# Kernel optimization log

Measured on AMD Instinct MI355X. Metric: run time of the kernel, lower is better.

Reference implementation:

```python
import jax, jax.numpy as jnp
import numpy as np

N = 262144
FEAT = 128
HID = 256


def setup_inputs() -> dict:
    key = jax.random.key(0)
    ks = jax.random.split(key, 6)
    rotation = jax.random.normal(ks[0], (N, 3, 3), dtype=jnp.float32)
    feature = jax.random.normal(ks[1], (N, FEAT), dtype=jnp.float32)
    # MLP params (scaled like default init)
    W1 = jax.random.normal(ks[2], (FEAT, HID), dtype=jnp.float32) / np.sqrt(FEAT)
    b1 = jnp.zeros((HID,), dtype=jnp.float32)
    W2 = jax.random.normal(ks[3], (HID, HID), dtype=jnp.float32) / np.sqrt(HID)
    b2 = jnp.zeros((HID,), dtype=jnp.float32)
    W3 = jax.random.normal(ks[4], (HID, 9), dtype=jnp.float32) / np.sqrt(HID)
    b3 = jnp.zeros((9,), dtype=jnp.float32)
    return {"rotation": rotation, "feature": feature,
            "W1": W1, "b1": b1, "W2": W2, "b2": b2, "W3": W3, "b3": b3}


def _mlp(feature, W1, b1, W2, b2, W3, b3):
    h = jax.nn.relu(feature @ W1 + b1)
    h = jax.nn.relu(h @ W2 + b2)
    return h @ W3 + b3  # [N, 9]


def reference(rotation, feature, W1, b1, W2, b2, W3, b3):
    # mat = net(feature).reshape(-1,3,3) + I
    mat = _mlp(feature, W1, b1, W2, b2, W3, b3).reshape(-1, 3, 3) + jnp.eye(3, dtype=rotation.dtype)
    # new_mat = mat @ rotation, then Procrustes projection via SVD: U @ V^T
    new_mat = jnp.einsum('nab,nbc->nac', mat, rotation)
    U, S, Vh = jnp.linalg.svd(new_mat, full_matrices=False)
    out = jnp.einsum('nab,nbc->nac', U, Vh)  # torch: U @ V.T == U @ Vh
    logdet = jnp.zeros((rotation.shape[0],), dtype=rotation.dtype)
    return out, logdet
```

## Files before the change

kernel.cpp:

```cpp
#include <hip/hip_runtime.h>
#include <math.h>


#define N_ROWS 262144
#define FEAT   128
#define HID    256
#define TM     64
#define NT     256
#define NBLK   (N_ROWS/TM)

typedef _Float16 h8v __attribute__((ext_vector_type(8)));
typedef float    f4v __attribute__((ext_vector_type(4)));

#define WS_W1H 0
#define WS_W1L 65536
#define WS_W2H 131072
#define WS_W2L 262144

#define OFF_AH  0
#define OFF_AL  16384
#define OFF_H1H 0
#define OFF_H1L 32768
#define W3SEC   2320
#define OFF_W3  65536
#define OFF_B3  (OFF_W3 + 4*W3SEC)
#define OFF_RS  (OFF_B3 + 64)
#define OFF_MS  (OFF_RS + TM*12*4)
#define SMEM_SZ (OFF_MS + TM*12*4)

__device__ __forceinline__ unsigned short hbits(_Float16 h) {
    return __builtin_bit_cast(unsigned short, h);
}

__global__ __launch_bounds__(256)
void prep_weights(const float* __restrict__ W1, const float* __restrict__ W2,
                  unsigned char* __restrict__ ws) {
    int e = blockIdx.x * 256 + threadIdx.x;
    unsigned short* w1h = (unsigned short*)(ws + WS_W1H);
    unsigned short* w1l = (unsigned short*)(ws + WS_W1L);
    unsigned short* w2h = (unsigned short*)(ws + WS_W2H);
    unsigned short* w2l = (unsigned short*)(ws + WS_W2L);
    if (e < FEAT * HID) {
        int j = e & 7, lane = (e >> 3) & 63, cb = (e >> 9) & 15, ks = e >> 13;
        int k = ks * 32 + ((lane >> 4) << 3) + j, n = cb * 16 + (lane & 15);
        float v = W1[k * HID + n];
        _Float16 h = (_Float16)v, l = (_Float16)(v - (float)h);
        w1h[e] = hbits(h); w1l[e] = hbits(l);
    } else if (e < FEAT * HID + HID * HID) {
        int e2 = e - FEAT * HID;
        int j = e2 & 7, lane = (e2 >> 3) & 63, cb = (e2 >> 9) & 15, ks = e2 >> 13;
        int k = ks * 32 + ((lane >> 4) << 3) + j, n = cb * 16 + (lane & 15);
        float v = W2[k * HID + n];
        _Float16 h = (_Float16)v, l = (_Float16)(v - (float)h);
        w2h[e2] = hbits(h); w2l[e2] = hbits(l);
    }
}

template<int KSTEPS, int ROWSTRIDE>
__device__ __forceinline__ void mfma_layer(const unsigned char* AH, const unsigned char* AL,
                                           const h8v* __restrict__ BH, const h8v* __restrict__ BL,
                                           f4v acc[4][4], int lane, int qc) {
#pragma unroll 2
    for (int ks = 0; ks < KSTEPS; ++ks) {
        h8v ah[4], al[4];
#pragma unroll
        for (int rt = 0; rt < 4; ++rt) {
            int row = rt * 16 + (lane & 15);
            unsigned byt = (unsigned)(row * ROWSTRIDE + ks * 64 + ((lane >> 4) << 4));
            byt ^= (unsigned)((row & 7) << 4);
            ah[rt] = *(const h8v*)(AH + byt);
            al[rt] = *(const h8v*)(AL + byt);
        }
#pragma unroll
        for (int ct = 0; ct < 4; ++ct) {
            int fi = ((ks * 16 + qc * 4 + ct) << 6) + lane;
            h8v bh = BH[fi], bl = BL[fi];
#pragma unroll
            for (int rt = 0; rt < 4; ++rt) {
                acc[rt][ct] = __builtin_amdgcn_mfma_f32_16x16x32_f16(ah[rt], bh, acc[rt][ct], 0, 0, 0);
                acc[rt][ct] = __builtin_amdgcn_mfma_f32_16x16x32_f16(ah[rt], bl, acc[rt][ct], 0, 0, 0);
                acc[rt][ct] = __builtin_amdgcn_mfma_f32_16x16x32_f16(al[rt], bh, acc[rt][ct], 0, 0, 0);
            }
        }
    }
}

__global__ __launch_bounds__(NT, 2)
void fused_main(const float* __restrict__ rot, const float* __restrict__ feat,
                const float* __restrict__ b1, const float* __restrict__ b2,
                const float* __restrict__ W3, const float* __restrict__ b3,
                const unsigned char* __restrict__ ws, float* __restrict__ out) {
    __shared__ __align__(16) unsigned char smem[SMEM_SZ];
    const int tid = threadIdx.x, lane = tid & 63, w = tid >> 6;
    const int row0 = blockIdx.x * TM;

    {
        const float4* f4 = (const float4*)(feat + (size_t)row0 * FEAT);
        for (int t = tid; t < TM * FEAT / 4; t += NT) {
            float4 v = f4[t];
            int row = t >> 5, c4 = t & 31;
            unsigned byt = (unsigned)(row * 256 + c4 * 8) ^ (unsigned)((row & 7) << 4);
            _Float16 h0 = (_Float16)v.x, h1v = (_Float16)v.y, h2v = (_Float16)v.z, h3v = (_Float16)v.w;
            _Float16 l0 = (_Float16)(v.x - (float)h0), l1v = (_Float16)(v.y - (float)h1v);
            _Float16 l2v = (_Float16)(v.z - (float)h2v), l3v = (_Float16)(v.w - (float)h3v);
            uint2 hp, lp;
            hp.x = (unsigned)hbits(h0)  | ((unsigned)hbits(h1v) << 16);
            hp.y = (unsigned)hbits(h2v) | ((unsigned)hbits(h3v) << 16);
            lp.x = (unsigned)hbits(l0)  | ((unsigned)hbits(l1v) << 16);
            lp.y = (unsigned)hbits(l2v) | ((unsigned)hbits(l3v) << 16);
            *(uint2*)(smem + OFF_AH + byt) = hp;
            *(uint2*)(smem + OFF_AL + byt) = lp;
        }
        for (int t = tid; t < HID * 9; t += NT) {
            int c = t / 9, o = t - 9 * c;
            *(float*)(smem + OFF_W3 + (c >> 6) * W3SEC + (c & 63) * 36 + o * 4) = W3[t];
        }
        if (tid < 9) ((float*)(smem + OFF_B3))[tid] = b3[tid];
        float* Rs = (float*)(smem + OFF_RS);
        for (int t = tid; t < TM * 9; t += NT)
            Rs[(t / 9) * 12 + (t % 9)] = rot[(size_t)row0 * 9 + t];
    }
    __syncthreads();

    f4v acc[4][4];
#pragma unroll
    for (int i = 0; i < 4; ++i)
#pragma unroll
        for (int j = 0; j < 4; ++j) acc[i][j] = (f4v)0.0f;
    mfma_layer<4, 256>(smem + OFF_AH, smem + OFF_AL,
                       (const h8v*)(ws + WS_W1H), (const h8v*)(ws + WS_W1L), acc, lane, w);
    __syncthreads();
#pragma unroll
    for (int ct = 0; ct < 4; ++ct) {
        int col = (w * 4 + ct) * 16 + (lane & 15);
        float bias = b1[col];
#pragma unroll
        for (int rt = 0; rt < 4; ++rt)
#pragma unroll
            for (int r = 0; r < 4; ++r) {
                int row = rt * 16 + ((lane >> 4) << 2) + r;
                float v = fmaxf(acc[rt][ct][r] + bias, 0.0f);
                _Float16 h = (_Float16)v, l = (_Float16)(v - (float)h);
                unsigned byt = (unsigned)(row * 512 + col * 2) ^ (unsigned)((row & 7) << 4);
                *(unsigned short*)(smem + OFF_H1H + byt) = hbits(h);
                *(unsigned short*)(smem + OFF_H1L + byt) = hbits(l);
            }
    }
    __syncthreads();

#pragma unroll
    for (int i = 0; i < 4; ++i)
#pragma unroll
        for (int j = 0; j < 4; ++j) acc[i][j] = (f4v)0.0f;
    mfma_layer<8, 512>(smem + OFF_H1H, smem + OFF_H1L,
                       (const h8v*)(ws + WS_W2H), (const h8v*)(ws + WS_W2L), acc, lane, w);
    __syncthreads();
#pragma unroll
    for (int ct = 0; ct < 4; ++ct) {
        int col = (w * 4 + ct) * 16 + (lane & 15);
        float bias = b2[col];
#pragma unroll
        for (int rt = 0; rt < 4; ++rt)
#pragma unroll
            for (int r = 0; r < 4; ++r) {
                int row = rt * 16 + ((lane >> 4) << 2) + r;
                unsigned byt = (unsigned)(row * 1024 + col * 4) ^ (unsigned)((row & 7) << 4);
                *(float*)(smem + byt) = fmaxf(acc[rt][ct][r] + bias, 0.0f);
            }
    }
    __syncthreads();

    const int r3 = (w << 4) + (lane & 15), kg = lane >> 4;
    float p[9];
#pragma unroll
    for (int o = 0; o < 9; ++o) p[o] = 0.0f;
#pragma unroll 4
    for (int j = 0; j < 16; ++j) {
        int col = kg * 64 + j * 4;
        unsigned byt = (unsigned)(r3 * 1024 + col * 4) ^ (unsigned)((r3 & 7) << 4);
        float4 h = *(const float4*)(smem + byt);
        const float* wrow = (const float*)(smem + OFF_W3 + kg * W3SEC + (j * 4) * 36);
#pragma unroll
        for (int e = 0; e < 4; ++e) {
            float hv = (e == 0) ? h.x : (e == 1) ? h.y : (e == 2) ? h.z : h.w;
            const float* wr = wrow + e * 9;
#pragma unroll
            for (int o = 0; o < 9; ++o) p[o] += hv * wr[o];
        }
    }
#pragma unroll
    for (int o = 0; o < 9; ++o) {
        p[o] += __shfl_xor(p[o], 16);
        p[o] += __shfl_xor(p[o], 32);
    }

    {
        float* Rs = (float*)(smem + OFF_RS);
        float* Ms = (float*)(smem + OFF_MS);
        const float* b3s = (const float*)(smem + OFF_B3);
        if (kg == 0) {
            const int r = r3;
            const float m0 = p[0] + b3s[0] + 1.0f, m1 = p[1] + b3s[1],        m2 = p[2] + b3s[2];
            const float m3 = p[3] + b3s[3],        m4 = p[4] + b3s[4] + 1.0f, m5 = p[5] + b3s[5];
            const float m6 = p[6] + b3s[6],        m7 = p[7] + b3s[7],        m8 = p[8] + b3s[8] + 1.0f;
            const float r0 = Rs[r*12+0], r1 = Rs[r*12+1], r2 = Rs[r*12+2];
            const float r3v = Rs[r*12+3], r4 = Rs[r*12+4], r5 = Rs[r*12+5];
            const float r6 = Rs[r*12+6], r7 = Rs[r*12+7], r8 = Rs[r*12+8];

            float x0 = m0*r0 + m1*r3v + m2*r6;
            float x1 = m0*r1 + m1*r4  + m2*r7;
            float x2 = m0*r2 + m1*r5  + m2*r8;
            float x3 = m3*r0 + m4*r3v + m5*r6;
            float x4 = m3*r1 + m4*r4  + m5*r7;
            float x5 = m3*r2 + m4*r5  + m5*r8;
            float x6 = m6*r0 + m7*r3v + m8*r6;
            float x7 = m6*r1 + m7*r4  + m8*r7;
            float x8 = m6*r2 + m7*r5  + m8*r8;

#pragma unroll 1
            for (int it = 0; it < 16; ++it) {
                const float c0 = x4*x8 - x5*x7;
                const float c1 = x5*x6 - x3*x8;
                const float c2 = x3*x7 - x4*x6;
                const float c3 = x2*x7 - x1*x8;
                const float c4 = x0*x8 - x2*x6;
                const float c5 = x1*x6 - x0*x7;
                const float c6 = x1*x5 - x2*x4;
                const float c7 = x2*x3 - x0*x5;
                const float c8 = x0*x4 - x1*x3;
                const float det = x0*c0 + x1*c1 + x2*c2;
                const float ad  = fmaxf(fabsf(det), 1e-30f);
                const float mu  = 1.0f / cbrtf(ad);
                const float dsafe = copysignf(ad, det);
                const float s1 = 0.5f * mu;
                const float s2 = 0.5f / (mu * dsafe);
                x0 = s1*x0 + s2*c0;  x1 = s1*x1 + s2*c1;  x2 = s1*x2 + s2*c2;
                x3 = s1*x3 + s2*c3;  x4 = s1*x4 + s2*c4;  x5 = s1*x5 + s2*c5;
                x6 = s1*x6 + s2*c6;  x7 = s1*x7 + s2*c7;  x8 = s1*x8 + s2*c8;
            }
            Ms[r*12+0] = x0; Ms[r*12+1] = x1; Ms[r*12+2] = x2;
            Ms[r*12+3] = x3; Ms[r*12+4] = x4; Ms[r*12+5] = x5;
            Ms[r*12+6] = x6; Ms[r*12+7] = x7; Ms[r*12+8] = x8;
        }
    }
    __syncthreads();

    {
        float* Ms = (float*)(smem + OFF_MS);
        for (int t = tid; t < TM * 9; t += NT)
            out[(size_t)row0 * 9 + t] = Ms[(t / 9) * 12 + (t % 9)];
        for (int t = tid; t < TM; t += NT)
            out[(size_t)N_ROWS * 9 + row0 + t] = 0.0f;
    }
}

extern "C" void kernel_launch(void* const* d_in, const int* in_sizes, int n_in,
                              void* d_out, int out_size, void* d_ws, size_t ws_size,
                              hipStream_t stream) {
    const float* rot  = (const float*)d_in[0];
    const float* feat = (const float*)d_in[1];
    const float* W1   = (const float*)d_in[2];
    const float* b1   = (const float*)d_in[3];
    const float* W2   = (const float*)d_in[4];
    const float* b2   = (const float*)d_in[5];
    const float* W3   = (const float*)d_in[6];
    const float* b3   = (const float*)d_in[7];
    float* out = (float*)d_out;
    unsigned char* ws = (unsigned char*)d_ws;
    (void)in_sizes; (void)n_in; (void)out_size; (void)ws_size;

    hipLaunchKernelGGL(prep_weights, dim3(384), dim3(256), 0, stream, W1, W2, ws);
    hipLaunchKernelGGL(fused_main, dim3(NBLK), dim3(NT), 0, stream,
                       rot, feat, b1, b2, W3, b3, ws, out);
}
```

Before: 423.8 us.

## Double waves per block, halve column tiles per wave, vectorize weight prep

```diff
diff --git a/kernel.cpp b/kernel.cpp
--- a/kernel.cpp
+++ b/kernel.cpp
@@ -6,7 +6,7 @@
 #define FEAT   128
 #define HID    256
 #define TM     64
-#define NT     256
+#define NT     512
 #define NBLK   (N_ROWS/TM)
 
 typedef _Float16 h8v __attribute__((ext_vector_type(8)));
@@ -21,9 +21,9 @@
 #define OFF_AL  16384
 #define OFF_H1H 0
 #define OFF_H1L 32768
-#define W3SEC   2320
+#define W3SEC   1168
 #define OFF_W3  65536
-#define OFF_B3  (OFF_W3 + 4*W3SEC)
+#define OFF_B3  (OFF_W3 + 8*W3SEC)
 #define OFF_RS  (OFF_B3 + 64)
 #define OFF_MS  (OFF_RS + TM*12*4)
 #define SMEM_SZ (OFF_MS + TM*12*4)
@@ -35,33 +35,39 @@
 __global__ __launch_bounds__(256)
 void prep_weights(const float* __restrict__ W1, const float* __restrict__ W2,
                   unsigned char* __restrict__ ws) {
-    int e = blockIdx.x * 256 + threadIdx.x;
-    unsigned short* w1h = (unsigned short*)(ws + WS_W1H);
-    unsigned short* w1l = (unsigned short*)(ws + WS_W1L);
-    unsigned short* w2h = (unsigned short*)(ws + WS_W2H);
-    unsigned short* w2l = (unsigned short*)(ws + WS_W2L);
-    if (e < FEAT * HID) {
-        int j = e & 7, lane = (e >> 3) & 63, cb = (e >> 9) & 15, ks = e >> 13;
-        int k = ks * 32 + ((lane >> 4) << 3) + j, n = cb * 16 + (lane & 15);
-        float v = W1[k * HID + n];
+    int g = blockIdx.x * 256 + threadIdx.x;
+    int base = g * 8;
+    const float* W; unsigned short* dh; unsigned short* dl; int e;
+    if (base < FEAT * HID) {
+        W = W1; dh = (unsigned short*)(ws + WS_W1H); dl = (unsigned short*)(ws + WS_W1L); e = base;
+    } else if (base < FEAT * HID + HID * HID) {
+        W = W2; dh = (unsigned short*)(ws + WS_W2H); dl = (unsigned short*)(ws + WS_W2L); e = base - FEAT * HID;
+    } else return;
+    int fl = (e >> 3) & 63, cb = (e >> 9) & 15, ks = e >> 13;
+    int k0 = ks * 32 + ((fl >> 4) << 3), n = cb * 16 + (fl & 15);
+    unsigned short hs[8], ls[8];
+#pragma unroll
+    for (int j = 0; j < 8; ++j) {
+        float v = W[(size_t)(k0 + j) * HID + n];
         _Float16 h = (_Float16)v, l = (_Float16)(v - (float)h);
-        w1h[e] = hbits(h); w1l[e] = hbits(l);
-    } else if (e < FEAT * HID + HID * HID) {
-        int e2 = e - FEAT * HID;
-        int j = e2 & 7, lane = (e2 >> 3) & 63, cb = (e2 >> 9) & 15, ks = e2 >> 13;
-        int k = ks * 32 + ((lane >> 4) << 3) + j, n = cb * 16 + (lane & 15);
-        float v = W2[k * HID + n];
-        _Float16 h = (_Float16)v, l = (_Float16)(v - (float)h);
-        w2h[e2] = hbits(h); w2l[e2] = hbits(l);
-    }
+        hs[j] = hbits(h); ls[j] = hbits(l);
+    }
+    *(uint4*)(dh + e) = *(const uint4*)hs;
+    *(uint4*)(dl + e) = *(const uint4*)ls;
 }
 
 template<int KSTEPS, int ROWSTRIDE>
 __device__ __forceinline__ void mfma_layer(const unsigned char* AH, const unsigned char* AL,
                                            const h8v* __restrict__ BH, const h8v* __restrict__ BL,
-                                           f4v acc[4][4], int lane, int qc) {
-#pragma unroll 2
+                                           f4v acc[4][2], int lane, int qc) {
+#pragma unroll
     for (int ks = 0; ks < KSTEPS; ++ks) {
+        h8v bh[2], bl[2];
+#pragma unroll
+        for (int ct = 0; ct < 2; ++ct) {
+            int fi = ((ks * 16 + qc * 2 + ct) << 6) + lane;
+            bh[ct] = BH[fi]; bl[ct] = BL[fi];
+        }
         h8v ah[4], al[4];
 #pragma unroll
         for (int rt = 0; rt < 4; ++rt) {
@@ -72,20 +78,17 @@
             al[rt] = *(const h8v*)(AL + byt);
         }
 #pragma unroll
-        for (int ct = 0; ct < 4; ++ct) {
-            int fi = ((ks * 16 + qc * 4 + ct) << 6) + lane;
-            h8v bh = BH[fi], bl = BL[fi];
+        for (int ct = 0; ct < 2; ++ct)
 #pragma unroll
             for (int rt = 0; rt < 4; ++rt) {
-                acc[rt][ct] = __builtin_amdgcn_mfma_f32_16x16x32_f16(ah[rt], bh, acc[rt][ct], 0, 0, 0);
-                acc[rt][ct] = __builtin_amdgcn_mfma_f32_16x16x32_f16(ah[rt], bl, acc[rt][ct], 0, 0, 0);
-                acc[rt][ct] = __builtin_amdgcn_mfma_f32_16x16x32_f16(al[rt], bh, acc[rt][ct], 0, 0, 0);
-            }
-        }
-    }
-}
-
-__global__ __launch_bounds__(NT, 2)
+                acc[rt][ct] = __builtin_amdgcn_mfma_f32_16x16x32_f16(ah[rt], bh[ct], acc[rt][ct], 0, 0, 0);
+                acc[rt][ct] = __builtin_amdgcn_mfma_f32_16x16x32_f16(ah[rt], bl[ct], acc[rt][ct], 0, 0, 0);
+                acc[rt][ct] = __builtin_amdgcn_mfma_f32_16x16x32_f16(al[rt], bh[ct], acc[rt][ct], 0, 0, 0);
+            }
+    }
+}
+
+__global__ __launch_bounds__(NT, 4)
 void fused_main(const float* __restrict__ rot, const float* __restrict__ feat,
                 const float* __restrict__ b1, const float* __restrict__ b2,
                 const float* __restrict__ W3, const float* __restrict__ b3,
@@ -96,7 +99,9 @@
 
     {
         const float4* f4 = (const float4*)(feat + (size_t)row0 * FEAT);
-        for (int t = tid; t < TM * FEAT / 4; t += NT) {
+#pragma unroll
+        for (int it = 0; it < TM * FEAT / 4 / NT; ++it) {
+            int t = it * NT + tid;
             float4 v = f4[t];
             int row = t >> 5, c4 = t & 31;
             unsigned byt = (unsigned)(row * 256 + c4 * 8) ^ (unsigned)((row & 7) << 4);
@@ -113,7 +118,7 @@
         }
         for (int t = tid; t < HID * 9; t += NT) {
             int c = t / 9, o = t - 9 * c;
-            *(float*)(smem + OFF_W3 + (c >> 6) * W3SEC + (c & 63) * 36 + o * 4) = W3[t];
+            *(float*)(smem + OFF_W3 + (c >> 5) * W3SEC + (c & 31) * 36 + o * 4) = W3[t];
         }
         if (tid < 9) ((float*)(smem + OFF_B3))[tid] = b3[tid];
         float* Rs = (float*)(smem + OFF_RS);
@@ -122,17 +127,17 @@
     }
     __syncthreads();
 
-    f4v acc[4][4];
+    f4v acc[4][2];
 #pragma unroll
     for (int i = 0; i < 4; ++i)
 #pragma unroll
-        for (int j = 0; j < 4; ++j) acc[i][j] = (f4v)0.0f;
+        for (int j = 0; j < 2; ++j) acc[i][j] = (f4v)0.0f;
     mfma_layer<4, 256>(smem + OFF_AH, smem + OFF_AL,
                        (const h8v*)(ws + WS_W1H), (const h8v*)(ws + WS_W1L), acc, lane, w);
     __syncthreads();
 #pragma unroll
-    for (int ct = 0; ct < 4; ++ct) {
-        int col = (w * 4 + ct) * 16 + (lane & 15);
+    for (int ct = 0; ct < 2; ++ct) {
+        int col = (w * 2 + ct) * 16 + (lane & 15);
         float bias = b1[col];
 #pragma unroll
         for (int rt = 0; rt < 4; ++rt)
@@ -151,13 +156,13 @@
 #pragma unroll
     for (int i = 0; i < 4; ++i)
 #pragma unroll
-        for (int j = 0; j < 4; ++j) acc[i][j] = (f4v)0.0f;
+        for (int j = 0; j < 2; ++j) acc[i][j] = (f4v)0.0f;
     mfma_layer<8, 512>(smem + OFF_H1H, smem + OFF_H1L,
                        (const h8v*)(ws + WS_W2H), (const h8v*)(ws + WS_W2L), acc, lane, w);
     __syncthreads();
 #pragma unroll
-    for (int ct = 0; ct < 4; ++ct) {
-        int col = (w * 4 + ct) * 16 + (lane & 15);
+    for (int ct = 0; ct < 2; ++ct) {
+        int col = (w * 2 + ct) * 16 + (lane & 15);
         float bias = b2[col];
 #pragma unroll
         for (int rt = 0; rt < 4; ++rt)
@@ -170,13 +175,13 @@
     }
     __syncthreads();
 
-    const int r3 = (w << 4) + (lane & 15), kg = lane >> 4;
+    const int r3 = (w << 3) + (lane & 7), kg = lane >> 3;
     float p[9];
 #pragma unroll
     for (int o = 0; o < 9; ++o) p[o] = 0.0f;
 #pragma unroll 4
-    for (int j = 0; j < 16; ++j) {
-        int col = kg * 64 + j * 4;
+    for (int j = 0; j < 8; ++j) {
+        int col = kg * 32 + j * 4;
         unsigned byt = (unsigned)(r3 * 1024 + col * 4) ^ (unsigned)((r3 & 7) << 4);
         float4 h = *(const float4*)(smem + byt);
         const float* wrow = (const float*)(smem + OFF_W3 + kg * W3SEC + (j * 4) * 36);
@@ -190,6 +195,7 @@
     }
 #pragma unroll
     for (int o = 0; o < 9; ++o) {
+        p[o] += __shfl_xor(p[o], 8);
         p[o] += __shfl_xor(p[o], 16);
         p[o] += __shfl_xor(p[o], 32);
     }
@@ -269,7 +275,7 @@
     unsigned char* ws = (unsigned char*)d_ws;
     (void)in_sizes; (void)n_in; (void)out_size; (void)ws_size;
 
-    hipLaunchKernelGGL(prep_weights, dim3(384), dim3(256), 0, stream, W1, W2, ws);
+    hipLaunchKernelGGL(prep_weights, dim3(48), dim3(256), 0, stream, W1, W2, ws);
     hipLaunchKernelGGL(fused_main, dim3(NBLK), dim3(NT), 0, stream,
                        rot, feat, b1, b2, W3, b3, ws, out);
 }
```

Result: no change. 424.9 us (+0.3%).
